# Kernel optimization log

Hardware: AMD Instinct MI355X
Metric: run time of the kernel (lower is better)

## Reference

```python
import jax, jax.numpy as jnp
import numpy as np

N, C_IN, HF, WF = 4, 256, 128, 128
IMG_H, IMG_W = 1024, 1024
A = 3  # anchors per location (1 size x 3 aspect ratios), matches RPNHead
OBJ_THR, IOU_THR = 0.3, 0.7
PRE_NMS, POST_NMS = 2000, 300  # pre-NMS top-k (== top_k_proposals_training), post-NMS top-k (testing)


def setup_inputs() -> dict:
    key = jax.random.key(0)
    ks = jax.random.split(key, 5)
    return {
        "feat": jax.random.normal(ks[0], (N, C_IN, HF, WF), jnp.float32),
        "conv_w": jax.random.normal(ks[1], (256, C_IN, 3, 3), jnp.float32) * 0.02,
        "conv_b": jnp.zeros((256,), jnp.float32),
        "det_w": jax.random.normal(ks[2], (A, 256, 1, 1), jnp.float32) * 0.05,
        "det_b": jnp.zeros((A,), jnp.float32),
        "reg_w": jax.random.normal(ks[3], (4 * A, 256, 1, 1), jnp.float32) * 0.02,
        "reg_b": jnp.zeros((4 * A,), jnp.float32),
    }


def _conv(x, w, b, pad):
    y = jax.lax.conv_general_dilated(x, w, (1, 1), [(pad, pad), (pad, pad)],
                                     dimension_numbers=("NCHW", "OIHW", "NCHW"))
    return y + b[None, :, None, None]


def _anchors():
    # AnchorGenerator.generate_anchors + grid_anchors, stride = image // grid
    scales = jnp.array([128.0], jnp.float32)
    ratios = jnp.array([0.5, 1.0, 2.0], jnp.float32)
    hr = jnp.sqrt(ratios)
    wr = 1.0 / hr
    ws = (wr[:, None] * scales[None, :]).reshape(-1)
    hs = (hr[:, None] * scales[None, :]).reshape(-1)
    base = jnp.round(jnp.stack([-ws, -hs, ws, hs], axis=1) / 2.0)  # [A,4]
    sx = jnp.arange(WF, dtype=jnp.float32) * (IMG_W // WF)
    sy = jnp.arange(HF, dtype=jnp.float32) * (IMG_H // HF)
    yy, xx = jnp.meshgrid(sy, sx, indexing="ij")
    shifts = jnp.stack([xx.ravel(), yy.ravel(), xx.ravel(), yy.ravel()], axis=1)  # [H*W,4]
    return (shifts[:, None, :] + base[None, :, :]).reshape(-1, 4)  # [H*W*A,4]


def _decode(anchors, deltas):
    # Faithful to source, including the x/y swap in the anchor-center computation.
    x1, y1, x2, y2 = anchors[..., 0], anchors[..., 1], anchors[..., 2], anchors[..., 3]
    aw = x2 - x1
    ah = y2 - y1
    acx = y1 + aw / 2  # (sic) matches original code
    acy = x1 + ah / 2  # (sic)
    dx, dy, dw, dh = deltas[..., 0], deltas[..., 1], deltas[..., 2], deltas[..., 3]
    px = acx + dx * aw
    py = acy + dy * ah
    pw = aw * jnp.exp(dw)
    ph = ah * jnp.exp(dh)
    return jnp.stack([px - pw / 2, py - ph / 2, px + pw / 2, py + ph / 2], axis=-1)


def _filter_one(boxes, scores):
    # clip -> degenerate filter -> objectness threshold -> NMS -> top-k, fixed shapes
    w = boxes[:, 2] - boxes[:, 0]
    h = boxes[:, 3] - boxes[:, 1]
    valid = (scores > OBJ_THR) & (w > 0) & (h > 0)
    s = jnp.where(valid, scores, -jnp.inf)
    top_s, top_i = jax.lax.top_k(s, PRE_NMS)
    b = boxes[top_i]
    v = valid[top_i]
    area = jnp.maximum(b[:, 2] - b[:, 0], 0) * jnp.maximum(b[:, 3] - b[:, 1], 0)
    ix1 = jnp.maximum(b[:, None, 0], b[None, :, 0])
    iy1 = jnp.maximum(b[:, None, 1], b[None, :, 1])
    ix2 = jnp.minimum(b[:, None, 2], b[None, :, 2])
    iy2 = jnp.minimum(b[:, None, 3], b[None, :, 3])
    inter = jnp.maximum(ix2 - ix1, 0) * jnp.maximum(iy2 - iy1, 0)
    iou = inter / jnp.maximum(area[:, None] + area[None, :] - inter, 1e-9)
    idxs = jnp.arange(PRE_NMS)

    def body(keep, i):
        sup = jnp.any((iou[i] > IOU_THR) & keep & (idxs < i))
        return keep.at[i].set(v[i] & ~sup), None

    keep, _ = jax.lax.scan(body, jnp.zeros(PRE_NMS, bool), idxs)
    fs = jnp.where(keep, top_s, -jnp.inf)
    sel_s, sel_i = jax.lax.top_k(fs, POST_NMS)
    kept = keep[sel_i]
    out = jnp.concatenate([b[sel_i], sel_s[:, None]], axis=-1)  # [POST,5] = box + score
    return jnp.where(kept[:, None], out, 0.0)


def reference(feat, conv_w, conv_b, det_w, det_b, reg_w, reg_b):
    x = _conv(feat, conv_w, conv_b, 1)                      # fpn conv 3x3, no activation
    obj = jax.nn.sigmoid(_conv(x, det_w, det_b, 0)).reshape(N, -1)  # [N, A*H*W]
    d = _conv(x, reg_w, reg_b, 0)                           # [N, 4A, H, W]
    d = d.reshape(N, 4, A, HF, WF).transpose(0, 2, 3, 4, 1).reshape(N, -1, 4)
    anchors = _anchors()                                    # [A_total, 4]
    props = _decode(anchors[None], d)
    props = jnp.stack([
        jnp.clip(props[..., 0], 0, IMG_W), jnp.clip(props[..., 1], 0, IMG_H),
        jnp.clip(props[..., 2], 0, IMG_W), jnp.clip(props[..., 3], 0, IMG_H)], axis=-1)
    return jax.vmap(_filter_one)(props, obj)  # [N, POST_NMS, 5]
```

## Files before the change

### kernel.cpp

```cpp
#include <hip/hip_runtime.h>
#include <hip/hip_bf16.h>
#include <hip/hip_fp16.h>
#include <stdint.h>
#include <math.h>

#define N_IMG 4
#define CIN 256
#define HFD 128
#define WFD 128
#define HW (HFD*WFD)
#define NA 3
#define NPROP (NA*HW)
#define PRE_NMS 2000
#define POST_NMS 300

__device__ __forceinline__ unsigned long long rl64(unsigned long long v, int i) {
    unsigned int lo = (unsigned int)__builtin_amdgcn_readlane((int)(unsigned int)v, i);
    unsigned int hi = (unsigned int)__builtin_amdgcn_readlane((int)(unsigned int)(v >> 32), i);
    return ((unsigned long long)hi << 32) | (unsigned long long)lo;
}

__device__ __forceinline__ double sum4(const double* __restrict__ PART, size_t cp) {
    const size_t S = (size_t)1 << 20;
    return (PART[cp] + PART[cp + S]) + (PART[cp + 2 * S] + PART[cp + 3 * S]);
}

__device__ __forceinline__ void decode_box(int i, double dx, double dy, double dwv, double dhv,
                                           double& c1o, double& c2o, double& c3o, double& c4o) {
    int loc = i / 3, aa = i % 3;
    int hh = loc >> 7, wwi = loc & 127;
    double sx = (double)(wwi * 8), sy = (double)(hh * 8);
    double bx1 = (aa == 0) ? -91.0 : (aa == 1 ? -64.0 : -45.0);
    double by1 = (aa == 0) ? -45.0 : (aa == 1 ? -64.0 : -91.0);
    double x1 = sx + bx1, y1 = sy + by1, x2 = sx - bx1, y2 = sy - by1;
    double aw = x2 - x1, ahh = y2 - y1;
    double acx = y1 + aw * 0.5;
    double acy = x1 + ahh * 0.5;
    double px = acx + dx * aw, py = acy + dy * ahh;
    double pw = aw * exp(dwv), ph = ahh * exp(dhv);
    double c1 = px - pw * 0.5, c2 = py - ph * 0.5, c3 = px + pw * 0.5, c4 = py + ph * 0.5;
    c1o = fmin(fmax(c1, 0.0), 1024.0);
    c2o = fmin(fmax(c2, 0.0), 1024.0);
    c3o = fmin(fmax(c3, 0.0), 1024.0);
    c4o = fmin(fmax(c4, 0.0), 1024.0);
}

__global__ __launch_bounds__(256) void k_effw64(const float* __restrict__ cw, const float* __restrict__ cb,
                                                const float* __restrict__ dw_, const float* __restrict__ db_,
                                                const float* __restrict__ rw_, const float* __restrict__ rb_,
                                                double* __restrict__ E64, double* __restrict__ EB64,
                                                unsigned long long* __restrict__ PSPREF,
                                                int* __restrict__ PSNEED,
                                                uint32_t* __restrict__ HIST,
                                                uint32_t* __restrict__ CNT)
{
    int b = blockIdx.x;
    int tid = threadIdx.x;
    if (b < 144) {
        __shared__ float hwl[15][260];
        __shared__ float wt[256][16];
        int k0 = b * 16;
        for (int idx = tid; idx < 15 * 256; idx += 256) {
            int c = idx >> 8, co = idx & 255;
            hwl[c][co] = (c < 3) ? dw_[c * 256 + co] : rw_[(c - 3) * 256 + co];
        }
        for (int idx = tid; idx < 4096; idx += 256) {
            int co = idx >> 4, kk = idx & 15;
            wt[co][kk] = cw[co * 2304 + k0 + kk];
        }
        __syncthreads();
        int kk = tid >> 4, c = tid & 15;
        double s = 0.0;
        if (c < 15) {
#pragma unroll 4
            for (int co = 0; co < 256; co++) s += (double)hwl[c][co] * (double)wt[co][kk];
        }
        E64[(k0 + kk) * 16 + c] = s;
    } else {
        if (tid < 16) {
            int c = tid;
            double s = 0.0; double hb = 0.0;
            if (c < 15) {
                const float* hw = (c < 3) ? (dw_ + c * 256) : (rw_ + (c - 3) * 256);
                for (int co = 0; co < 256; co++) s += (double)hw[co] * (double)cb[co];
                hb = (double)((c < 3) ? db_[c] : rb_[c - 3]);
            }
            EB64[c] = s + hb;
        }
        for (int i = tid; i < N_IMG * 2048; i += 256) HIST[i] = 0u;
        if (tid < N_IMG) { PSPREF[tid] = 0ull; PSNEED[tid] = PRE_NMS; CNT[tid] = 0u; }
    }
}

__global__ __launch_bounds__(256, 4) void k_conv64(const float* __restrict__ feat,
                                                   const double* __restrict__ E64,
                                                   double* __restrict__ PART)
{
    __shared__ float in_t[8][4][136];
    int b = blockIdx.x;
    int chunk = b & 3; int hp = (b >> 2) & 63; int n = b >> 8;
    int h0 = hp * 2;
    int tid = threadIdx.x;
    int q = tid & 63;
    int row = q >> 5, qq = q & 31, w0 = qq * 4;
    int g = tid >> 6;
    double acc[4][4];
#pragma unroll
    for (int cc = 0; cc < 4; cc++)
#pragma unroll
        for (int px = 0; px < 4; px++) acc[cc][px] = 0.0;

    for (int sl = 0; sl < 8; sl++) {
        int ci0 = (chunk << 6) + sl * 8;
        for (int t = tid; t < 1024; t += 256) {
            int seg = t & 31;
            int rid = t >> 5;
            int ci = rid >> 2, dr = rid & 3;
            int gh = h0 - 1 + dr;
            float4 v = make_float4(0.f, 0.f, 0.f, 0.f);
            if (gh >= 0 && gh < HFD)
                v = *(const float4*)&feat[(((size_t)((n << 8) + ci0 + ci)) << 14) + (gh << 7) + (seg << 2)];
            *(float4*)&in_t[ci][dr][4 + (seg << 2)] = v;
        }
        __syncthreads();
        for (int ci = 0; ci < 8; ci++) {
            int kbase = ((ci0 + ci) * 9) << 4;
#pragma unroll
            for (int r = 0; r < 3; r++) {
                float4 f4 = *(const float4*)&in_t[ci][row + r][4 + w0];
                float left   = __shfl_up(f4.w, 1);
                float right1 = __shfl_down(f4.x, 1);
                if (qq == 0)  left   = 0.f;
                if (qq == 31) right1 = 0.f;
                double fv[6];
                fv[0] = (double)left;
                fv[1] = (double)f4.x; fv[2] = (double)f4.y;
                fv[3] = (double)f4.z; fv[4] = (double)f4.w;
                fv[5] = (double)right1;
#pragma unroll
                for (int s = 0; s < 3; s++) {
                    int widx = __builtin_amdgcn_readfirstlane(kbase + (((r * 3 + s) << 4) + (g << 2)));
                    const double* wp = E64 + widx;
                    double2 wv0 = *(const double2*)(wp);
                    double2 wv1 = *(const double2*)(wp + 2);
#pragma unroll
                    for (int px = 0; px < 4; px++) {
                        double f = fv[s + px];
                        acc[0][px] += wv0.x * f;
                        acc[1][px] += wv0.y * f;
                        acc[2][px] += wv1.x * f;
                        acc[3][px] += wv1.y * f;
                    }
                }
            }
        }
        __syncthreads();
    }
    int gpos = (n << 14) + ((h0 + row) << 7) + w0;
    double* base = PART + ((size_t)chunk << 20) + gpos;
#pragma unroll
    for (int cc = 0; cc < 4; cc++) {
        int c = g * 4 + cc;
        if (c < 15) {
            double2 s0; s0.x = acc[cc][0]; s0.y = acc[cc][1];
            double2 s1; s1.x = acc[cc][2]; s1.y = acc[cc][3];
            *(double2*)(base + (size_t)c * 65536) = s0;
            *(double2*)(base + (size_t)c * 65536 + 2) = s1;
        }
    }
}

__global__ __launch_bounds__(256) void k_findecode(const double* __restrict__ PART,
                                                   const double* __restrict__ EB64,
                                                   unsigned long long* __restrict__ KEY64,
                                                   uint32_t* __restrict__ HIST)
{
    __shared__ uint32_t h2[2048];
    int tid = threadIdx.x;
    for (int i = tid; i < 2048; i += 256) h2[i] = 0u;
    __syncthreads();
    int p = blockIdx.x * 256 + tid;
    int n = p >> 14, pos = p & 16383;
    double L[15];
#pragma unroll
    for (int c = 0; c < 15; c++)
        L[c] = sum4(PART, (size_t)c * 65536 + p) + EB64[c];
#pragma unroll
    for (int a = 0; a < 3; a++) {
        double logit = L[a];
        double score = 1.0 / (1.0 + exp(-logit));
        int i = a * HW + pos;
        double c1, c2, c3, c4;
        decode_box(i, L[3 + a], L[6 + a], L[9 + a], L[12 + a], c1, c2, c3, c4);
        bool valid = (score > 0.3) && (c3 - c1 > 0.0) && (c4 - c2 > 0.0);
        unsigned long long key = valid ? ~((unsigned long long)__double_as_longlong(score)) : ~0ull;
        KEY64[(size_t)n * NPROP + i] = key;
        atomicAdd(&h2[(uint32_t)(key >> 53)], 1u);
    }
    __syncthreads();
    uint32_t* G = HIST + n * 2048;
    for (int i = tid; i < 2048; i += 256) {
        uint32_t v = h2[i];
        if (v) atomicAdd(&G[i], v);
    }
}

__global__ __launch_bounds__(256) void k_hist(const unsigned long long* __restrict__ KEY64,
                                              const unsigned long long* __restrict__ PSPREF,
                                              uint32_t* __restrict__ HIST, int L)
{
    __shared__ uint32_t h[2048];
    int blk = blockIdx.x; int n = blk >> 4, sub = blk & 15;
    int tid = threadIdx.x;
    for (int i = tid; i < 2048; i += 256) h[i] = 0u;
    __syncthreads();
    int sh = 53 - 11 * L;
    unsigned long long pref = PSPREF[n];
    const unsigned long long* K = KEY64 + (size_t)n * NPROP + sub * 3072;
    for (int i = tid; i < 3072; i += 256) {
        unsigned long long k = K[i];
        if ((k >> (sh + 11)) == pref) atomicAdd(&h[(uint32_t)((k >> sh) & 2047ull)], 1u);
    }
    __syncthreads();
    uint32_t* G = HIST + n * 2048;
    for (int i = tid; i < 2048; i += 256) {
        uint32_t v = h[i];
        if (v) atomicAdd(&G[i], v);
    }
}

__global__ __launch_bounds__(256) void k_pick(uint32_t* __restrict__ HIST,
                                              unsigned long long* __restrict__ PSPREF,
                                              int* __restrict__ PSNEED)
{
    int n = blockIdx.x; int tid = threadIdx.x;
    __shared__ uint32_t hl[2048];
    __shared__ uint32_t psum[256];
    uint32_t* G = HIST + n * 2048;
    for (int i = tid; i < 2048; i += 256) hl[i] = G[i];
    __syncthreads();
    {
        uint32_t s = 0;
        for (int qq = 0; qq < 8; qq++) s += hl[tid * 8 + qq];
        psum[tid] = s;
    }
    __syncthreads();
    if (tid == 0) {
        int need = PSNEED[n];
        unsigned long long pref = PSPREF[n];
        uint32_t cum = 0; int g = 255;
        for (int t = 0; t < 256; t++) { uint32_t c = psum[t]; if (cum + c >= (uint32_t)need) { g = t; break; } cum += c; }
        int bsel = g * 8 + 7;
        for (int t = g * 8; t < g * 8 + 8; t++) { uint32_t c = hl[t]; if (cum + c >= (uint32_t)need) { bsel = t; break; } cum += c; }
        PSNEED[n] = need - (int)cum;
        PSPREF[n] = (pref << 11) | (unsigned long long)bsel;
    }
    __syncthreads();
    for (int i = tid; i < 2048; i += 256) G[i] = 0u;
}

__global__ __launch_bounds__(256) void k_collect(const unsigned long long* __restrict__ KEY64,
                                                 const unsigned long long* __restrict__ PSPREF,
                                                 uint32_t* __restrict__ CNT,
                                                 unsigned long long* __restrict__ CANDK,
                                                 uint32_t* __restrict__ CANDI)
{
    int blk = blockIdx.x; int n = blk >> 4, sub = blk & 15;
    int tid = threadIdx.x;
    unsigned long long pref44 = PSPREF[n];
    const unsigned long long* K = KEY64 + (size_t)n * NPROP;
    int base = sub * 3072;
    for (int i = tid; i < 3072; i += 256) {
        unsigned long long k = K[base + i];
        if (k != ~0ull && (k >> 20) <= pref44) {
            uint32_t p2 = atomicAdd(&CNT[n], 1u);
            if (p2 < 2048u) { CANDK[n * 2048 + p2] = k; CANDI[n * 2048 + p2] = (uint32_t)(base + i); }
        }
    }
}

__global__ __launch_bounds__(1024) void k_finalsel(const uint32_t* __restrict__ CNT,
                                                   const unsigned long long* __restrict__ CANDK,
                                                   const uint32_t* __restrict__ CANDI,
                                                   const double* __restrict__ PART,
                                                   const double* __restrict__ EB64,
                                                   unsigned long long* __restrict__ skeys,
                                                   double* __restrict__ bsort,
                                                   double* __restrict__ area)
{
    int n = blockIdx.x; int tid = threadIdx.x;
    __shared__ unsigned long long selk[2048];
    __shared__ uint32_t seli[2048];
    uint32_t cnt = CNT[n]; if (cnt > 2048u) cnt = 2048u;
    for (int t = tid; t < 2048; t += 1024) {
        if (t < (int)cnt) { selk[t] = CANDK[n * 2048 + t]; seli[t] = CANDI[n * 2048 + t]; }
        else { selk[t] = ~0ull; seli[t] = 0xFFFFFFFFu; }
    }
    __syncthreads();
    for (unsigned k2 = 2; k2 <= 2048; k2 <<= 1) {
        for (unsigned jx = k2 >> 1; jx > 0; jx >>= 1) {
            for (int t = tid; t < 2048; t += 1024) {
                unsigned ixj = (unsigned)t ^ jx;
                if (ixj > (unsigned)t) {
                    bool up = ((t & k2) == 0);
                    unsigned long long ka = selk[t], kb = selk[ixj];
                    uint32_t ia = seli[t], ib = seli[ixj];
                    bool agt = (ka > kb) || (ka == kb && ia > ib);
                    if (up ? agt : !agt) {
                        selk[t] = kb; selk[ixj] = ka;
                        seli[t] = ib; seli[ixj] = ia;
                    }
                }
            }
            __syncthreads();
        }
    }
    for (int t = tid; t < 2048; t += 1024) {
        bool valid = (t < PRE_NMS) && (selk[t] != ~0ull);
        if (t < PRE_NMS) skeys[(size_t)n * PRE_NMS + t] = valid ? selk[t] : ~0ull;
        double b0 = 0, b1 = 0, b2 = 0, b3 = 0;
        if (valid) {
            int i = (int)seli[t];
            int a = i >> 14, pos = i & 16383;
            size_t p = ((size_t)n << 14) + pos;
            double dx  = sum4(PART, (size_t)(3 + a)  * 65536 + p) + EB64[3 + a];
            double dy  = sum4(PART, (size_t)(6 + a)  * 65536 + p) + EB64[6 + a];
            double dwv = sum4(PART, (size_t)(9 + a)  * 65536 + p) + EB64[9 + a];
            double dhv = sum4(PART, (size_t)(12 + a) * 65536 + p) + EB64[12 + a];
            decode_box(i, dx, dy, dwv, dhv, b0, b1, b2, b3);
        }
        double* bs = bsort + (((size_t)(n * 2048 + t)) << 2);
        bs[0] = b0; bs[1] = b1; bs[2] = b2; bs[3] = b3;
        area[(size_t)n * 2048 + t] = fmax(b2 - b0, 0.0) * fmax(b3 - b1, 0.0);
    }
}

__global__ __launch_bounds__(256) void k_iou2(const double* __restrict__ bsort,
                                              const double* __restrict__ area,
                                              unsigned long long* __restrict__ mat)
{
    int blk = blockIdx.x; int n = blk >> 6; int rt = blk & 63;
    int tid = threadIdx.x;
    int r = tid >> 3, g = tid & 7;
    int i = rt * 32 + r;
    const double* bp = bsort + ((size_t)n * 2048 + i) * 4;
    double bx0 = bp[0], bx1_ = bp[1], bx2_ = bp[2], bx3 = bp[3];
    double ai = area[(size_t)n * 2048 + i];
    __shared__ double cbx[512][4];
    __shared__ double ca[512];
    for (int cc = 0; cc < 4; cc++) {
        if ((cc + 1) * 512 <= rt * 32) continue;
        __syncthreads();
        for (int idx = tid; idx < 512; idx += 256) {
            const double* sp = bsort + ((size_t)n * 2048 + cc * 512 + idx) * 4;
            cbx[idx][0] = sp[0]; cbx[idx][1] = sp[1]; cbx[idx][2] = sp[2]; cbx[idx][3] = sp[3];
            ca[idx] = area[(size_t)n * 2048 + cc * 512 + idx];
        }
        __syncthreads();
        unsigned long long wd = 0ull;
        for (int jb = 0; jb < 64; jb++) {
            int jr = (jb + g * 9) & 63;
            int jj = g * 64 + jr;
            double ix1 = fmax(bx0, cbx[jj][0]);
            double iy1 = fmax(bx1_, cbx[jj][1]);
            double ix2 = fmin(bx2_, cbx[jj][2]);
            double iy2 = fmin(bx3, cbx[jj][3]);
            double inter = fmax(ix2 - ix1, 0.0) * fmax(iy2 - iy1, 0.0);
            double den = fmax(ai + ca[jj] - inter, 1e-9);
            double iou = inter / den;
            if (iou > 0.7) wd |= (1ull << jr);
        }
        mat[((size_t)n * 2048 + i) * 32 + cc * 8 + g] = wd;
    }
}

__global__ __launch_bounds__(256) void k_nms3(const unsigned long long* __restrict__ skeys,
                                              const double* __restrict__ bsort,
                                              const unsigned long long* __restrict__ mat,
                                              float* __restrict__ out)
{
    int n = blockIdx.x; int tid = threadIdx.x;
    int lane = tid & 63;
    __shared__ unsigned long long rb[2][64][33];
    __shared__ unsigned long long sup_lds[32];
    __shared__ unsigned long long vb[32];
    __shared__ unsigned long long kbw[32];
    __shared__ int s_stop;
    float* dout = out + n * (POST_NMS * 5);
    for (int t = tid; t < POST_NMS * 5; t += 256) dout[t] = 0.f;
    if (tid < 32) { sup_lds[tid] = 0ull; kbw[tid] = 0ull; }
    if (tid == 0) s_stop = 0;
    if (tid < 64) {
        for (int i0 = 0; i0 < 2048; i0 += 64) {
            int i = i0 + lane;
            unsigned long long k = (i < PRE_NMS) ? skeys[(size_t)n * PRE_NMS + i] : ~0ull;
            unsigned long long m = __ballot(k != ~0ull);
            if (lane == 0) vb[i0 >> 6] = m;
        }
    }
    int r = tid >> 2, w0 = (tid & 3) * 8;
    {
        const unsigned long long* src = mat + ((size_t)n * 2048 + r) * 32 + w0;
        ulonglong2 a = *(const ulonglong2*)(src);
        ulonglong2 b = *(const ulonglong2*)(src + 2);
        ulonglong2 c2 = *(const ulonglong2*)(src + 4);
        ulonglong2 d = *(const ulonglong2*)(src + 6);
        unsigned long long* dst = &rb[0][r][w0];
        dst[0] = a.x; dst[1] = a.y; dst[2] = b.x; dst[3] = b.y;
        dst[4] = c2.x; dst[5] = c2.y; dst[6] = d.x; dst[7] = d.y;
    }
    __syncthreads();
    int total_kept = 0;
    for (int c = 0; c < 32; c++) {
        if (s_stop) break;
        int cur = c & 1, nxt = cur ^ 1;
        ulonglong2 pa, pb, pc, pd;
        bool pf = (c + 1 < 32);
        if (pf) {
            const unsigned long long* src = mat + ((size_t)n * 2048 + (c + 1) * 64 + r) * 32 + w0;
            pa = *(const ulonglong2*)(src);
            pb = *(const ulonglong2*)(src + 2);
            pc = *(const ulonglong2*)(src + 4);
            pd = *(const ulonglong2*)(src + 6);
        }
        if (tid < 64) {
            unsigned long long M = rb[cur][lane][c];
            unsigned long long supw = sup_lds[c];
            unsigned long long vbw = vb[c];
            unsigned long long km = 0ull;
#pragma unroll
            for (int ii = 0; ii < 64; ii++) {
                unsigned long long bit = 1ull << ii;
                if ((vbw & bit) && !(supw & bit)) {
                    km |= bit;
                    supw |= rl64(M, ii);
                }
            }
            if (lane == 0) {
                kbw[c] = km;
                total_kept += __popcll(km);
                if (total_kept >= POST_NMS) s_stop = 1;
            }
        }
        __syncthreads();
        {
            int w = tid & 31, g = tid >> 5;
            unsigned long long km2 = kbw[c];
            unsigned long long sub = (km2 >> (g * 8)) & 0xFFull;
            unsigned long long acc = 0ull;
            while (sub) {
                int bpos = __ffsll((long long)sub) - 1;
                sub &= sub - 1;
                acc |= rb[cur][g * 8 + bpos][w];
            }
            if (acc) atomicOr(&sup_lds[w], acc);
        }
        if (pf) {
            unsigned long long* dst = &rb[nxt][r][w0];
            dst[0] = pa.x; dst[1] = pa.y; dst[2] = pb.x; dst[3] = pb.y;
            dst[4] = pc.x; dst[5] = pc.y; dst[6] = pd.x; dst[7] = pd.y;
        }
        __syncthreads();
    }
    if (tid < 64) {
        int running = 0;
        for (int i0 = 0; i0 < 2048; i0 += 64) {
            int i = i0 + lane;
            bool kp = (i < PRE_NMS) && ((kbw[i >> 6] >> (i & 63)) & 1ull);
            unsigned long long m = __ballot(kp);
            if (kp) {
                int rk = running + __popcll(m & ((1ull << lane) - 1ull));
                if (rk < POST_NMS) {
                    const double* bp2 = bsort + ((size_t)n * 2048 + i) * 4;
                    unsigned long long k = skeys[(size_t)n * PRE_NMS + i];
                    double s = __longlong_as_double((long long)~k);
                    float* o = dout + rk * 5;
                    o[0] = (float)bp2[0]; o[1] = (float)bp2[1];
                    o[2] = (float)bp2[2]; o[3] = (float)bp2[3];
                    o[4] = (float)s;
                }
            }
            running += __popcll(m);
        }
    }
}

extern "C" void kernel_launch(void* const* d_in, const int* in_sizes, int n_in,
                              void* d_out, int out_size, void* d_ws, size_t ws_size,
                              hipStream_t stream) {
    (void)in_sizes; (void)n_in; (void)out_size; (void)ws_size;
    const float* feat   = (const float*)d_in[0];
    const float* conv_w = (const float*)d_in[1];
    const float* conv_b = (const float*)d_in[2];
    const float* det_w  = (const float*)d_in[3];
    const float* det_b  = (const float*)d_in[4];
    const float* reg_w  = (const float*)d_in[5];
    const float* reg_b  = (const float*)d_in[6];
    float* out = (float*)d_out;

    char* w = (char*)d_ws;
    double* E64 = (double*)w;                          w += (size_t)2304 * 16 * 8;
    double* EB64 = (double*)w;                         w += 128;
    double* PART = (double*)w;                         w += (size_t)4 << 23;
    unsigned long long* KEY64 = (unsigned long long*)w; w += (size_t)N_IMG * NPROP * 8;
    unsigned long long* PSPREF = (unsigned long long*)w; w += N_IMG * 8;
    int* PSNEED = (int*)w;                             w += 64;
    uint32_t* HIST = (uint32_t*)w;                     w += (size_t)N_IMG * 2048 * 4;
    uint32_t* CNT = (uint32_t*)w;                      w += 64;
    unsigned long long* CANDK = (unsigned long long*)w; w += (size_t)N_IMG * 2048 * 8;
    uint32_t* CANDI = (uint32_t*)w;                    w += (size_t)N_IMG * 2048 * 4;
    unsigned long long* SKEY = (unsigned long long*)w; w += (size_t)N_IMG * PRE_NMS * 8;
    double* BSORT = (double*)w;                        w += (size_t)N_IMG * 2048 * 4 * 8;
    double* AREA = (double*)w;                         w += (size_t)N_IMG * 2048 * 8;
    unsigned long long* MAT = (unsigned long long*)w;  w += (size_t)N_IMG * 2048 * 32 * 8;

    k_effw64<<<dim3(145), dim3(256), 0, stream>>>(conv_w, conv_b, det_w, det_b, reg_w, reg_b,
                                                  E64, EB64, PSPREF, PSNEED, HIST, CNT);
    k_conv64<<<dim3(1024), dim3(256), 0, stream>>>(feat, E64, PART);
    k_findecode<<<dim3(256), dim3(256), 0, stream>>>(PART, EB64, KEY64, HIST);
    k_pick<<<dim3(N_IMG), dim3(256), 0, stream>>>(HIST, PSPREF, PSNEED);
    for (int L = 1; L < 4; L++) {
        k_hist<<<dim3(64), dim3(256), 0, stream>>>(KEY64, PSPREF, HIST, L);
        k_pick<<<dim3(N_IMG), dim3(256), 0, stream>>>(HIST, PSPREF, PSNEED);
    }
    k_collect<<<dim3(64), dim3(256), 0, stream>>>(KEY64, PSPREF, CNT, CANDK, CANDI);
    k_finalsel<<<dim3(N_IMG), dim3(1024), 0, stream>>>(CNT, CANDK, CANDI, PART, EB64, SKEY, BSORT, AREA);
    k_iou2<<<dim3(N_IMG * 64), dim3(256), 0, stream>>>(BSORT, AREA, MAT);
    k_nms3<<<dim3(N_IMG), dim3(256), 0, stream>>>(SKEY, BSORT, MAT, out);
}
```

Baseline: 374.8 us.

## Fuse radix-select stages into producer kernels via atomic completion counters

```diff
diff --git a/kernel.cpp b/kernel.cpp
--- a/kernel.cpp
+++ b/kernel.cpp
@@ -45,6 +45,40 @@
     c4o = fmin(fmax(c4, 0.0), 1024.0);
 }
 
+__device__ __forceinline__ void pick_one(uint32_t* __restrict__ G,
+                                         unsigned long long* __restrict__ PSPREF,
+                                         int* __restrict__ PSNEED, int n,
+                                         int tid, uint32_t* hl, uint32_t* psum) {
+    for (int i = tid; i < 2048; i += 256) hl[i] = G[i];
+    __syncthreads();
+    {
+        uint32_t s = 0;
+        for (int qq = 0; qq < 8; qq++) s += hl[tid * 8 + qq];
+        psum[tid] = s;
+    }
+    __syncthreads();
+    if (tid == 0) {
+        int need = PSNEED[n];
+        unsigned long long pref = PSPREF[n];
+        uint32_t cum = 0; int g = 255;
+        for (int t = 0; t < 256; t++) { uint32_t c = psum[t]; if (cum + c >= (uint32_t)need) { g = t; break; } cum += c; }
+        int bsel = g * 8 + 7;
+        for (int t = g * 8; t < g * 8 + 8; t++) { uint32_t c = hl[t]; if (cum + c >= (uint32_t)need) { bsel = t; break; } cum += c; }
+        PSNEED[n] = need - (int)cum;
+        PSPREF[n] = (pref << 11) | (unsigned long long)bsel;
+    }
+    __syncthreads();
+    for (int i = tid; i < 2048; i += 256) G[i] = 0u;
+}
+
+__device__ __forceinline__ void spin_until(uint32_t* __restrict__ ctr, uint32_t target, int tid) {
+    if (tid == 0) {
+        while (atomicAdd(ctr, 0u) < target) __builtin_amdgcn_s_sleep(1);
+    }
+    __syncthreads();
+    __threadfence();
+}
+
 __global__ __launch_bounds__(256) void k_effw64(const float* __restrict__ cw, const float* __restrict__ cb,
                                                 const float* __restrict__ dw_, const float* __restrict__ db_,
                                                 const float* __restrict__ rw_, const float* __restrict__ rb_,
@@ -52,7 +86,8 @@
                                                 unsigned long long* __restrict__ PSPREF,
                                                 int* __restrict__ PSNEED,
                                                 uint32_t* __restrict__ HIST,
-                                                uint32_t* __restrict__ CNT)
+                                                uint32_t* __restrict__ CNT,
+                                                uint32_t* __restrict__ DONE)
 {
     int b = blockIdx.x;
     int tid = threadIdx.x;
@@ -89,6 +124,7 @@
         }
         for (int i = tid; i < N_IMG * 2048; i += 256) HIST[i] = 0u;
         if (tid < N_IMG) { PSPREF[tid] = 0ull; PSNEED[tid] = PRE_NMS; CNT[tid] = 0u; }
+        if (tid < 8) DONE[tid] = 0u;
     }
 }
 
@@ -173,124 +209,122 @@
 __global__ __launch_bounds__(256) void k_findecode(const double* __restrict__ PART,
                                                    const double* __restrict__ EB64,
                                                    unsigned long long* __restrict__ KEY64,
-                                                   uint32_t* __restrict__ HIST)
+                                                   uint32_t* __restrict__ HIST,
+                                                   uint32_t* __restrict__ DONE,
+                                                   unsigned long long* __restrict__ PSPREF,
+                                                   int* __restrict__ PSNEED)
 {
     __shared__ uint32_t h2[2048];
+    __shared__ uint32_t psum[256];
     int tid = threadIdx.x;
-    for (int i = tid; i < 2048; i += 256) h2[i] = 0u;
-    __syncthreads();
-    int p = blockIdx.x * 256 + tid;
-    int n = p >> 14, pos = p & 16383;
-    double L[15];
-#pragma unroll
-    for (int c = 0; c < 15; c++)
-        L[c] = sum4(PART, (size_t)c * 65536 + p) + EB64[c];
-#pragma unroll
-    for (int a = 0; a < 3; a++) {
-        double logit = L[a];
-        double score = 1.0 / (1.0 + exp(-logit));
-        int i = a * HW + pos;
-        double c1, c2, c3, c4;
-        decode_box(i, L[3 + a], L[6 + a], L[9 + a], L[12 + a], c1, c2, c3, c4);
-        bool valid = (score > 0.3) && (c3 - c1 > 0.0) && (c4 - c2 > 0.0);
-        unsigned long long key = valid ? ~((unsigned long long)__double_as_longlong(score)) : ~0ull;
-        KEY64[(size_t)n * NPROP + i] = key;
-        atomicAdd(&h2[(uint32_t)(key >> 53)], 1u);
-    }
-    __syncthreads();
-    uint32_t* G = HIST + n * 2048;
-    for (int i = tid; i < 2048; i += 256) {
-        uint32_t v = h2[i];
-        if (v) atomicAdd(&G[i], v);
-    }
-}
-
-__global__ __launch_bounds__(256) void k_hist(const unsigned long long* __restrict__ KEY64,
-                                              const unsigned long long* __restrict__ PSPREF,
-                                              uint32_t* __restrict__ HIST, int L)
+    int blk = blockIdx.x;
+    if (blk < 256) {
+        for (int i = tid; i < 2048; i += 256) h2[i] = 0u;
+        __syncthreads();
+        int p = blk * 256 + tid;
+        int n = p >> 14, pos = p & 16383;
+        double L[15];
+#pragma unroll
+        for (int c = 0; c < 15; c++)
+            L[c] = sum4(PART, (size_t)c * 65536 + p) + EB64[c];
+#pragma unroll
+        for (int a = 0; a < 3; a++) {
+            double logit = L[a];
+            double score = 1.0 / (1.0 + exp(-logit));
+            int i = a * HW + pos;
+            double c1, c2, c3, c4;
+            decode_box(i, L[3 + a], L[6 + a], L[9 + a], L[12 + a], c1, c2, c3, c4);
+            bool valid = (score > 0.3) && (c3 - c1 > 0.0) && (c4 - c2 > 0.0);
+            unsigned long long key = valid ? ~((unsigned long long)__double_as_longlong(score)) : ~0ull;
+            KEY64[(size_t)n * NPROP + i] = key;
+            atomicAdd(&h2[(uint32_t)(key >> 53)], 1u);
+        }
+        __syncthreads();
+        uint32_t* G = HIST + n * 2048;
+        for (int i = tid; i < 2048; i += 256) {
+            uint32_t v = h2[i];
+            if (v) atomicAdd(&G[i], v);
+        }
+        __threadfence();
+        __syncthreads();
+        if (tid == 0) atomicAdd(&DONE[0], 1u);
+    } else {
+        int n = blk - 256;
+        spin_until(&DONE[0], 256u, tid);
+        pick_one(HIST + n * 2048, PSPREF, PSNEED, n, tid, h2, psum);
+    }
+}
+
+__global__ __launch_bounds__(256) void k_histpick(const unsigned long long* __restrict__ KEY64,
+                                                  unsigned long long* __restrict__ PSPREF,
+                                                  int* __restrict__ PSNEED,
+                                                  uint32_t* __restrict__ HIST,
+                                                  uint32_t* __restrict__ DONE, int L)
 {
     __shared__ uint32_t h[2048];
-    int blk = blockIdx.x; int n = blk >> 4, sub = blk & 15;
-    int tid = threadIdx.x;
-    for (int i = tid; i < 2048; i += 256) h[i] = 0u;
-    __syncthreads();
-    int sh = 53 - 11 * L;
-    unsigned long long pref = PSPREF[n];
-    const unsigned long long* K = KEY64 + (size_t)n * NPROP + sub * 3072;
-    for (int i = tid; i < 3072; i += 256) {
-        unsigned long long k = K[i];
-        if ((k >> (sh + 11)) == pref) atomicAdd(&h[(uint32_t)((k >> sh) & 2047ull)], 1u);
-    }
-    __syncthreads();
-    uint32_t* G = HIST + n * 2048;
-    for (int i = tid; i < 2048; i += 256) {
-        uint32_t v = h[i];
-        if (v) atomicAdd(&G[i], v);
-    }
-}
-
-__global__ __launch_bounds__(256) void k_pick(uint32_t* __restrict__ HIST,
-                                              unsigned long long* __restrict__ PSPREF,
-                                              int* __restrict__ PSNEED)
-{
-    int n = blockIdx.x; int tid = threadIdx.x;
-    __shared__ uint32_t hl[2048];
     __shared__ uint32_t psum[256];
-    uint32_t* G = HIST + n * 2048;
-    for (int i = tid; i < 2048; i += 256) hl[i] = G[i];
-    __syncthreads();
-    {
-        uint32_t s = 0;
-        for (int qq = 0; qq < 8; qq++) s += hl[tid * 8 + qq];
-        psum[tid] = s;
-    }
-    __syncthreads();
-    if (tid == 0) {
-        int need = PSNEED[n];
+    int blk = blockIdx.x; int tid = threadIdx.x;
+    if (blk < 64) {
+        int n = blk >> 4, sub = blk & 15;
+        for (int i = tid; i < 2048; i += 256) h[i] = 0u;
+        __syncthreads();
+        int sh = 53 - 11 * L;
         unsigned long long pref = PSPREF[n];
-        uint32_t cum = 0; int g = 255;
-        for (int t = 0; t < 256; t++) { uint32_t c = psum[t]; if (cum + c >= (uint32_t)need) { g = t; break; } cum += c; }
-        int bsel = g * 8 + 7;
-        for (int t = g * 8; t < g * 8 + 8; t++) { uint32_t c = hl[t]; if (cum + c >= (uint32_t)need) { bsel = t; break; } cum += c; }
-        PSNEED[n] = need - (int)cum;
-        PSPREF[n] = (pref << 11) | (unsigned long long)bsel;
-    }
-    __syncthreads();
-    for (int i = tid; i < 2048; i += 256) G[i] = 0u;
-}
-
-__global__ __launch_bounds__(256) void k_collect(const unsigned long long* __restrict__ KEY64,
-                                                 const unsigned long long* __restrict__ PSPREF,
-                                                 uint32_t* __restrict__ CNT,
-                                                 unsigned long long* __restrict__ CANDK,
-                                                 uint32_t* __restrict__ CANDI)
-{
-    int blk = blockIdx.x; int n = blk >> 4, sub = blk & 15;
-    int tid = threadIdx.x;
-    unsigned long long pref44 = PSPREF[n];
-    const unsigned long long* K = KEY64 + (size_t)n * NPROP;
-    int base = sub * 3072;
-    for (int i = tid; i < 3072; i += 256) {
-        unsigned long long k = K[base + i];
-        if (k != ~0ull && (k >> 20) <= pref44) {
-            uint32_t p2 = atomicAdd(&CNT[n], 1u);
-            if (p2 < 2048u) { CANDK[n * 2048 + p2] = k; CANDI[n * 2048 + p2] = (uint32_t)(base + i); }
-        }
-    }
-}
-
-__global__ __launch_bounds__(1024) void k_finalsel(const uint32_t* __restrict__ CNT,
-                                                   const unsigned long long* __restrict__ CANDK,
-                                                   const uint32_t* __restrict__ CANDI,
-                                                   const double* __restrict__ PART,
-                                                   const double* __restrict__ EB64,
-                                                   unsigned long long* __restrict__ skeys,
-                                                   double* __restrict__ bsort,
-                                                   double* __restrict__ area)
-{
-    int n = blockIdx.x; int tid = threadIdx.x;
+        const unsigned long long* K = KEY64 + (size_t)n * NPROP + sub * 3072;
+        for (int i = tid; i < 3072; i += 256) {
+            unsigned long long k = K[i];
+            if ((k >> (sh + 11)) == pref) atomicAdd(&h[(uint32_t)((k >> sh) & 2047ull)], 1u);
+        }
+        __syncthreads();
+        uint32_t* G = HIST + n * 2048;
+        for (int i = tid; i < 2048; i += 256) {
+            uint32_t v = h[i];
+            if (v) atomicAdd(&G[i], v);
+        }
+        __threadfence();
+        __syncthreads();
+        if (tid == 0) atomicAdd(&DONE[L], 1u);
+    } else {
+        int n = blk - 64;
+        spin_until(&DONE[L], 64u, tid);
+        pick_one(HIST + n * 2048, PSPREF, PSNEED, n, tid, h, psum);
+    }
+}
+
+__global__ __launch_bounds__(1024) void k_collectsel(const unsigned long long* __restrict__ KEY64,
+                                                     const unsigned long long* __restrict__ PSPREF,
+                                                     uint32_t* __restrict__ CNT,
+                                                     unsigned long long* __restrict__ CANDK,
+                                                     uint32_t* __restrict__ CANDI,
+                                                     uint32_t* __restrict__ DONE,
+                                                     const double* __restrict__ PART,
+                                                     const double* __restrict__ EB64,
+                                                     unsigned long long* __restrict__ skeys,
+                                                     double* __restrict__ bsort,
+                                                     double* __restrict__ area)
+{
     __shared__ unsigned long long selk[2048];
     __shared__ uint32_t seli[2048];
+    int blk = blockIdx.x; int tid = threadIdx.x;
+    if (blk < 64) {
+        int n = blk >> 4, sub = blk & 15;
+        unsigned long long pref44 = PSPREF[n];
+        const unsigned long long* K = KEY64 + (size_t)n * NPROP;
+        int base = sub * 3072;
+        for (int i = tid; i < 3072; i += 1024) {
+            unsigned long long k = K[base + i];
+            if (k != ~0ull && (k >> 20) <= pref44) {
+                uint32_t p2 = atomicAdd(&CNT[n], 1u);
+                if (p2 < 2048u) { CANDK[n * 2048 + p2] = k; CANDI[n * 2048 + p2] = (uint32_t)(base + i); }
+            }
+        }
+        __threadfence();
+        __syncthreads();
+        if (tid == 0) atomicAdd(&DONE[4], 1u);
+        return;
+    }
+    int n = blk - 64;
+    spin_until(&DONE[4], 64u, tid);
     uint32_t cnt = CNT[n]; if (cnt > 2048u) cnt = 2048u;
     for (int t = tid; t < 2048; t += 1024) {
         if (t < (int)cnt) { selk[t] = CANDK[n * 2048 + t]; seli[t] = CANDI[n * 2048 + t]; }
@@ -507,6 +541,7 @@
     int* PSNEED = (int*)w;                             w += 64;
     uint32_t* HIST = (uint32_t*)w;                     w += (size_t)N_IMG * 2048 * 4;
     uint32_t* CNT = (uint32_t*)w;                      w += 64;
+    uint32_t* DONE = (uint32_t*)w;                     w += 64;
     unsigned long long* CANDK = (unsigned long long*)w; w += (size_t)N_IMG * 2048 * 8;
     uint32_t* CANDI = (uint32_t*)w;                    w += (size_t)N_IMG * 2048 * 4;
     unsigned long long* SKEY = (unsigned long long*)w; w += (size_t)N_IMG * PRE_NMS * 8;
@@ -515,16 +550,14 @@
     unsigned long long* MAT = (unsigned long long*)w;  w += (size_t)N_IMG * 2048 * 32 * 8;
 
     k_effw64<<<dim3(145), dim3(256), 0, stream>>>(conv_w, conv_b, det_w, det_b, reg_w, reg_b,
-                                                  E64, EB64, PSPREF, PSNEED, HIST, CNT);
+                                                  E64, EB64, PSPREF, PSNEED, HIST, CNT, DONE);
     k_conv64<<<dim3(1024), dim3(256), 0, stream>>>(feat, E64, PART);
-    k_findecode<<<dim3(256), dim3(256), 0, stream>>>(PART, EB64, KEY64, HIST);
-    k_pick<<<dim3(N_IMG), dim3(256), 0, stream>>>(HIST, PSPREF, PSNEED);
+    k_findecode<<<dim3(260), dim3(256), 0, stream>>>(PART, EB64, KEY64, HIST, DONE, PSPREF, PSNEED);
     for (int L = 1; L < 4; L++) {
-        k_hist<<<dim3(64), dim3(256), 0, stream>>>(KEY64, PSPREF, HIST, L);
-        k_pick<<<dim3(N_IMG), dim3(256), 0, stream>>>(HIST, PSPREF, PSNEED);
-    }
-    k_collect<<<dim3(64), dim3(256), 0, stream>>>(KEY64, PSPREF, CNT, CANDK, CANDI);
-    k_finalsel<<<dim3(N_IMG), dim3(1024), 0, stream>>>(CNT, CANDK, CANDI, PART, EB64, SKEY, BSORT, AREA);
+        k_histpick<<<dim3(68), dim3(256), 0, stream>>>(KEY64, PSPREF, PSNEED, HIST, DONE, L);
+    }
+    k_collectsel<<<dim3(68), dim3(1024), 0, stream>>>(KEY64, PSPREF, CNT, CANDK, CANDI, DONE,
+                                                      PART, EB64, SKEY, BSORT, AREA);
     k_iou2<<<dim3(N_IMG * 64), dim3(256), 0, stream>>>(BSORT, AREA, MAT);
     k_nms3<<<dim3(N_IMG), dim3(256), 0, stream>>>(SKEY, BSORT, MAT, out);
 }
```

Measured after the change: 416.0 us. 1.11x slower.
